# Kernel tuning notes

Hardware: AMD Instinct MI355X
Metric: run time of the kernel (lower is better)

The kernel has to match this reference:

```python
import jax, jax.numpy as jnp
import numpy as np

MARGIN = 40.0


def setup_inputs() -> dict:
    key = jax.random.key(0)
    k1, k2 = jax.random.split(key)
    feat = jax.random.normal(k1, (4096, 512), dtype=jnp.float32)
    targets = jax.random.randint(k2, (4096,), 0, 64, dtype=jnp.int64)
    return {"feat": feat, "targets": targets}


def reference(feat, targets):
    # corr: (n, n) Gram matrix of features
    corr = feat @ feat.T
    # mask[i, j] = True if same class
    mask = targets[:, None] == targets[None, :]
    big = jnp.asarray(jnp.finfo(corr.dtype).max, corr.dtype)
    # per-row min over positives, max over negatives
    corr_ap = jnp.min(jnp.where(mask, corr, big), axis=1)
    corr_an = jnp.max(jnp.where(mask, -big, corr), axis=1)
    # MarginRankingLoss(margin=40) with y = 1: mean(relu(-(ap - an) + margin))
    loss = jnp.mean(jax.nn.relu(corr_an - corr_ap + MARGIN))
    return loss
```

## Files before the change

kernel.cpp:

```cpp
#include <hip/hip_runtime.h>
#include <float.h>
#include <stdint.h>


#define N_ROWS 4096
#define D_K    512
#define BT     128
#define BK     64
#define NTB    (N_ROWS / BT)
#define NTILES (NTB * (NTB + 1) / 2)
#define MARGIN 40.0f
#define FOLD_BLOCKS 16

typedef __bf16 bf16_t;
typedef bf16_t bf16x8 __attribute__((ext_vector_type(8)));
typedef float  floatx4 __attribute__((ext_vector_type(4)));
typedef unsigned short ushort_t;
typedef ushort_t ushortx8 __attribute__((ext_vector_type(8)));

#define GLOAD_LDS16(g, l)                                        \
    __builtin_amdgcn_global_load_lds(                            \
        (const __attribute__((address_space(1))) void*)(g),      \
        (__attribute__((address_space(3))) void*)(l), 16, 0, 0)

__device__ __forceinline__ ushort_t f2bf_rne(float x) {
    uint32_t u = __builtin_bit_cast(uint32_t, x);
    return (ushort_t)((u + 0x7FFFu + ((u >> 16) & 1u)) >> 16);
}

__global__ __launch_bounds__(256) void cast_kernel(
    const float* __restrict__ f, ushort_t* __restrict__ o,
    int* __restrict__ counter)
{
    const int gid = blockIdx.x * 256 + threadIdx.x;
    if (gid == 0) *counter = 0;

    const int i = gid * 8;
    const float4 v0 = *(const float4*)(f + i);
    const float4 v1 = *(const float4*)(f + i + 4);
    ushortx8 r;
    r[0] = f2bf_rne(v0.x); r[1] = f2bf_rne(v0.y);
    r[2] = f2bf_rne(v0.z); r[3] = f2bf_rne(v0.w);
    r[4] = f2bf_rne(v1.x); r[5] = f2bf_rne(v1.y);
    r[6] = f2bf_rne(v1.z); r[7] = f2bf_rne(v1.w);
    *(ushortx8*)(o + i) = r;
}

__global__ __launch_bounds__(512, 6) void gram_mfma_kernel(
    const ushort_t* __restrict__ fb, const int* __restrict__ tgt,
    float* __restrict__ ap_part, float* __restrict__ an_part)
{
    __shared__ __align__(16) ushort_t As[BT * BK];
    __shared__ __align__(16) ushort_t Bs[BT * BK];
    __shared__ int tgI[BT];
    __shared__ int tgJ[BT];

    float* apRed  = (float*)As;
    float* anRed  = apRed  + 4 * BT;
    float* apRedT = anRed  + 4 * BT;
    float* anRedT = apRedT + 2 * BT;

    int bi = 0, rem = blockIdx.x;
    while (rem >= NTB - bi) { rem -= NTB - bi; ++bi; }
    const int bj = bi + rem;

    const int tid  = threadIdx.x;
    const int i0   = bi * BT;
    const int j0   = bj * BT;
    const int lane = tid & 63;
    const int wave = tid >> 6;
    const int wr   = wave >> 2;
    const int wc   = wave & 3;
    const int lr   = lane & 15;
    const int lg   = lane >> 4;
    const int sw   = lr & 7;

    if (tid < BT)            tgI[tid]      = tgt[i0 + tid];
    else if (tid < 2 * BT)   tgJ[tid - BT] = tgt[j0 + tid - BT];

    const int srow = tid >> 3;
    const int schk = (tid & 7) ^ (srow & 7);
    const size_t gA0 = (size_t)(i0 + srow) * D_K + schk * 8;
    const size_t gB0 = (size_t)(j0 + srow) * D_K + schk * 8;
    const size_t gHi = (size_t)64 * D_K;
    char* AsB = (char*)As;
    char* BsB = (char*)Bs;

    floatx4 acc[4][2];
#pragma unroll
    for (int a = 0; a < 4; ++a)
#pragma unroll
        for (int b = 0; b < 2; ++b) acc[a][b] = (floatx4)0.0f;

    for (int k0 = 0; k0 < D_K; k0 += BK) {
        GLOAD_LDS16(fb + gA0 + k0,       AsB + tid * 16);
        GLOAD_LDS16(fb + gA0 + gHi + k0, AsB + 8192 + tid * 16);
        GLOAD_LDS16(fb + gB0 + k0,       BsB + tid * 16);
        GLOAD_LDS16(fb + gB0 + gHi + k0, BsB + 8192 + tid * 16);
        __syncthreads();

#pragma unroll
        for (int h = 0; h < 2; ++h) {
            bf16x8 af[4], bfr[2];
            const int pc = ((h * 4 + lg) ^ sw) * 8;
#pragma unroll
            for (int rg = 0; rg < 4; ++rg)
                af[rg] = *(const bf16x8*)(As + (wr * 64 + rg * 16 + lr) * BK + pc);
#pragma unroll
            for (int cg = 0; cg < 2; ++cg)
                bfr[cg] = *(const bf16x8*)(Bs + (wc * 32 + cg * 16 + lr) * BK + pc);
#pragma unroll
            for (int rg = 0; rg < 4; ++rg)
#pragma unroll
                for (int cg = 0; cg < 2; ++cg)
                    acc[rg][cg] = __builtin_amdgcn_mfma_f32_16x16x32_bf16(
                        af[rg], bfr[cg], acc[rg][cg], 0, 0, 0);
        }
        __syncthreads();
    }

    int tj[2];
#pragma unroll
    for (int cg = 0; cg < 2; ++cg) tj[cg] = tgJ[wc * 32 + cg * 16 + lr];

    float apT[2], anT[2];
#pragma unroll
    for (int cg = 0; cg < 2; ++cg) { apT[cg] = FLT_MAX; anT[cg] = -FLT_MAX; }

#pragma unroll
    for (int rg = 0; rg < 4; ++rg) {
#pragma unroll
        for (int r = 0; r < 4; ++r) {
            const int rloc = wr * 64 + rg * 16 + lg * 4 + r;
            const int ti = tgI[rloc];
            float vap = FLT_MAX, van = -FLT_MAX;
#pragma unroll
            for (int cg = 0; cg < 2; ++cg) {
                const float v = acc[rg][cg][r];
                if (ti == tj[cg]) { vap = fminf(vap, v); apT[cg] = fminf(apT[cg], v); }
                else              { van = fmaxf(van, v); anT[cg] = fmaxf(anT[cg], v); }
            }
#pragma unroll
            for (int m = 1; m < 16; m <<= 1) {
                vap = fminf(vap, __shfl_xor(vap, m));
                van = fmaxf(van, __shfl_xor(van, m));
            }
            if (lr == 0) { apRed[wc * BT + rloc] = vap; anRed[wc * BT + rloc] = van; }
        }
    }
#pragma unroll
    for (int cg = 0; cg < 2; ++cg) {
        float vap = apT[cg], van = anT[cg];
        vap = fminf(vap, __shfl_xor(vap, 16)); van = fmaxf(van, __shfl_xor(van, 16));
        vap = fminf(vap, __shfl_xor(vap, 32)); van = fmaxf(van, __shfl_xor(van, 32));
        if (lg == 0) {
            apRedT[wr * BT + wc * 32 + cg * 16 + lr] = vap;
            anRedT[wr * BT + wc * 32 + cg * 16 + lr] = van;
        }
    }
    __syncthreads();

    if (tid < BT) {
        const float ap = fminf(fminf(apRed[0 * BT + tid], apRed[1 * BT + tid]),
                               fminf(apRed[2 * BT + tid], apRed[3 * BT + tid]));
        const float an = fmaxf(fmaxf(anRed[0 * BT + tid], anRed[1 * BT + tid]),
                               fmaxf(anRed[2 * BT + tid], anRed[3 * BT + tid]));
        ap_part[(size_t)bj * N_ROWS + i0 + tid] = ap;
        an_part[(size_t)bj * N_ROWS + i0 + tid] = an;
        if (bi != bj) {
            ap_part[(size_t)bi * N_ROWS + j0 + tid] =
                fminf(apRedT[0 * BT + tid], apRedT[1 * BT + tid]);
            an_part[(size_t)bi * N_ROWS + j0 + tid] =
                fmaxf(anRedT[0 * BT + tid], anRedT[1 * BT + tid]);
        }
    }
}

__global__ __launch_bounds__(256) void fold_kernel(
    const float* __restrict__ ap_part, const float* __restrict__ an_part,
    float* __restrict__ blk_sum, int* __restrict__ counter,
    float* __restrict__ out)
{
    __shared__ float sred[4];
    const int tid = threadIdx.x;
    const int row = blockIdx.x * 256 + tid;
    const int lane = tid & 63;
    const int wave = tid >> 6;

    float ap = FLT_MAX, an = -FLT_MAX;
#pragma unroll 8
    for (int s = 0; s < NTB; ++s) {
        ap = fminf(ap, ap_part[(size_t)s * N_ROWS + row]);
        an = fmaxf(an, an_part[(size_t)s * N_ROWS + row]);
    }
    const float v = an - ap + MARGIN;
    float local = (v > 0.0f) ? v : 0.0f;
#pragma unroll
    for (int m = 32; m >= 1; m >>= 1) local += __shfl_down(local, m);
    if (lane == 0) sred[wave] = local;
    __syncthreads();

    if (tid == 0) {
        blk_sum[blockIdx.x] = sred[0] + sred[1] + sred[2] + sred[3];
        __threadfence();
        if (atomicAdd(counter, 1) == FOLD_BLOCKS - 1) {
            __threadfence();
            float s = 0.0f;
#pragma unroll
            for (int b = 0; b < FOLD_BLOCKS; ++b) s += blk_sum[b];
            out[0] = s * (1.0f / N_ROWS);
        }
    }
}

extern "C" void kernel_launch(void* const* d_in, const int* in_sizes, int n_in,
                              void* d_out, int out_size, void* d_ws, size_t ws_size,
                              hipStream_t stream)
{
    const float* feat = (const float*)d_in[0];
    const int*   tgt  = (const int*)d_in[1];

    ushort_t* fb      = (ushort_t*)d_ws;
    float*    ap_part = (float*)(fb + (size_t)N_ROWS * D_K);
    float*    an_part = ap_part + (size_t)NTB * N_ROWS;
    float*    blk_sum = an_part + (size_t)NTB * N_ROWS;
    int*      counter = (int*)(blk_sum + FOLD_BLOCKS);

    cast_kernel<<<(N_ROWS * D_K) / (256 * 8), 256, 0, stream>>>(feat, fb, counter);
    gram_mfma_kernel<<<NTILES, 512, 0, stream>>>(fb, tgt, ap_part, an_part);
    fold_kernel<<<FOLD_BLOCKS, 256, 0, stream>>>(ap_part, an_part, blk_sum,
                                                 counter, (float*)d_out);
}
```

Measured before the change: 86.40 us.

## Double-buffer LDS tiles and fold reduction into gram kernel via atomics

Double-buffers the A/B LDS tiles so the next K-slice's global-to-LDS loads are issued before the MFMAs on the current slice, leaving one barrier per iteration. It replaces the per-tile partial arrays and the separate fold kernel with monotonic-encoded atomicMin/atomicMax on per-row min/max. The last block, found through a global counter, computes the final loss. This doubles LDS use, lowers the occupancy hint from 6 to 4, and adds global atomics, but removes one kernel launch and the partial-array traffic.

Measured after the change: 95.54 us. +10.6%, slower.

```diff
diff --git a/kernel.cpp b/kernel.cpp
--- a/kernel.cpp
+++ b/kernel.cpp
@@ -9,8 +9,8 @@
 #define BK     64
 #define NTB    (N_ROWS / BT)
 #define NTILES (NTB * (NTB + 1) / 2)
+#define NITER  (D_K / BK)
 #define MARGIN 40.0f
-#define FOLD_BLOCKS 16
 
 typedef __bf16 bf16_t;
 typedef bf16_t bf16x8 __attribute__((ext_vector_type(8)));
@@ -28,12 +28,23 @@
     return (ushort_t)((u + 0x7FFFu + ((u >> 16) & 1u)) >> 16);
 }
 
+__device__ __forceinline__ unsigned int f2mono(float x) {
+    uint32_t u = __builtin_bit_cast(uint32_t, x);
+    return (u & 0x80000000u) ? ~u : (u | 0x80000000u);
+}
+__device__ __forceinline__ float mono2f(unsigned int m) {
+    uint32_t u = (m & 0x80000000u) ? (m ^ 0x80000000u) : ~m;
+    return __builtin_bit_cast(float, u);
+}
+
 __global__ __launch_bounds__(256) void cast_kernel(
     const float* __restrict__ f, ushort_t* __restrict__ o,
+    unsigned int* __restrict__ ap_m, unsigned int* __restrict__ an_m,
     int* __restrict__ counter)
 {
     const int gid = blockIdx.x * 256 + threadIdx.x;
     if (gid == 0) *counter = 0;
+    if (gid < N_ROWS) { ap_m[gid] = 0xFFFFFFFFu; an_m[gid] = 0u; }
 
     const int i = gid * 8;
     const float4 v0 = *(const float4*)(f + i);
@@ -46,14 +57,16 @@
     *(ushortx8*)(o + i) = r;
 }
 
-__global__ __launch_bounds__(512, 6) void gram_mfma_kernel(
+__global__ __launch_bounds__(512, 4) void gram_mfma_kernel(
     const ushort_t* __restrict__ fb, const int* __restrict__ tgt,
-    float* __restrict__ ap_part, float* __restrict__ an_part)
+    unsigned int* __restrict__ ap_m, unsigned int* __restrict__ an_m,
+    int* __restrict__ counter, float* __restrict__ out)
 {
-    __shared__ __align__(16) ushort_t As[BT * BK];
-    __shared__ __align__(16) ushort_t Bs[BT * BK];
+    __shared__ __align__(16) ushort_t As[2][BT * BK];
+    __shared__ __align__(16) ushort_t Bs[2][BT * BK];
     __shared__ int tgI[BT];
     __shared__ int tgJ[BT];
+    __shared__ int s_last;
 
     float* apRed  = (float*)As;
     float* anRed  = apRed  + 4 * BT;
@@ -83,8 +96,14 @@
     const size_t gA0 = (size_t)(i0 + srow) * D_K + schk * 8;
     const size_t gB0 = (size_t)(j0 + srow) * D_K + schk * 8;
     const size_t gHi = (size_t)64 * D_K;
-    char* AsB = (char*)As;
-    char* BsB = (char*)Bs;
+
+#define STAGE(buf, kk) do {                                          \
+        char* aD = (char*)As[buf]; char* bD = (char*)Bs[buf];        \
+        GLOAD_LDS16(fb + gA0 + (kk),       aD + tid * 16);           \
+        GLOAD_LDS16(fb + gA0 + gHi + (kk), aD + 8192 + tid * 16);    \
+        GLOAD_LDS16(fb + gB0 + (kk),       bD + tid * 16);           \
+        GLOAD_LDS16(fb + gB0 + gHi + (kk), bD + 8192 + tid * 16);    \
+    } while (0)
 
     floatx4 acc[4][2];
 #pragma unroll
@@ -92,23 +111,26 @@
 #pragma unroll
         for (int b = 0; b < 2; ++b) acc[a][b] = (floatx4)0.0f;
 
-    for (int k0 = 0; k0 < D_K; k0 += BK) {
-        GLOAD_LDS16(fb + gA0 + k0,       AsB + tid * 16);
-        GLOAD_LDS16(fb + gA0 + gHi + k0, AsB + 8192 + tid * 16);
-        GLOAD_LDS16(fb + gB0 + k0,       BsB + tid * 16);
-        GLOAD_LDS16(fb + gB0 + gHi + k0, BsB + 8192 + tid * 16);
-        __syncthreads();
-
+    STAGE(0, 0);
+    __syncthreads();
+
+    int cur = 0;
+#pragma unroll
+    for (int t = 0; t < NITER; ++t) {
+        if (t + 1 < NITER) STAGE(cur ^ 1, (t + 1) * BK);
+
+        const ushort_t* Acur = As[cur];
+        const ushort_t* Bcur = Bs[cur];
 #pragma unroll
         for (int h = 0; h < 2; ++h) {
             bf16x8 af[4], bfr[2];
             const int pc = ((h * 4 + lg) ^ sw) * 8;
 #pragma unroll
             for (int rg = 0; rg < 4; ++rg)
-                af[rg] = *(const bf16x8*)(As + (wr * 64 + rg * 16 + lr) * BK + pc);
+                af[rg] = *(const bf16x8*)(Acur + (wr * 64 + rg * 16 + lr) * BK + pc);
 #pragma unroll
             for (int cg = 0; cg < 2; ++cg)
-                bfr[cg] = *(const bf16x8*)(Bs + (wc * 32 + cg * 16 + lr) * BK + pc);
+                bfr[cg] = *(const bf16x8*)(Bcur + (wc * 32 + cg * 16 + lr) * BK + pc);
 #pragma unroll
             for (int rg = 0; rg < 4; ++rg)
 #pragma unroll
@@ -116,7 +138,10 @@
                     acc[rg][cg] = __builtin_amdgcn_mfma_f32_16x16x32_bf16(
                         af[rg], bfr[cg], acc[rg][cg], 0, 0, 0);
         }
-        __syncthreads();
+        if (t + 1 < NITER) {
+            __syncthreads();
+            cur ^= 1;
+        }
     }
 
     int tj[2];
@@ -165,52 +190,47 @@
                                fminf(apRed[2 * BT + tid], apRed[3 * BT + tid]));
         const float an = fmaxf(fmaxf(anRed[0 * BT + tid], anRed[1 * BT + tid]),
                                fmaxf(anRed[2 * BT + tid], anRed[3 * BT + tid]));
-        ap_part[(size_t)bj * N_ROWS + i0 + tid] = ap;
-        an_part[(size_t)bj * N_ROWS + i0 + tid] = an;
+        atomicMin(ap_m + i0 + tid, f2mono(ap));
+        atomicMax(an_m + i0 + tid, f2mono(an));
         if (bi != bj) {
-            ap_part[(size_t)bi * N_ROWS + j0 + tid] =
-                fminf(apRedT[0 * BT + tid], apRedT[1 * BT + tid]);
-            an_part[(size_t)bi * N_ROWS + j0 + tid] =
-                fmaxf(anRedT[0 * BT + tid], anRedT[1 * BT + tid]);
-        }
-    }
-}
-
-__global__ __launch_bounds__(256) void fold_kernel(
-    const float* __restrict__ ap_part, const float* __restrict__ an_part,
-    float* __restrict__ blk_sum, int* __restrict__ counter,
-    float* __restrict__ out)
-{
-    __shared__ float sred[4];
-    const int tid = threadIdx.x;
-    const int row = blockIdx.x * 256 + tid;
-    const int lane = tid & 63;
-    const int wave = tid >> 6;
-
-    float ap = FLT_MAX, an = -FLT_MAX;
-#pragma unroll 8
-    for (int s = 0; s < NTB; ++s) {
-        ap = fminf(ap, ap_part[(size_t)s * N_ROWS + row]);
-        an = fmaxf(an, an_part[(size_t)s * N_ROWS + row]);
-    }
-    const float v = an - ap + MARGIN;
-    float local = (v > 0.0f) ? v : 0.0f;
-#pragma unroll
-    for (int m = 32; m >= 1; m >>= 1) local += __shfl_down(local, m);
-    if (lane == 0) sred[wave] = local;
-    __syncthreads();
-
+            atomicMin(ap_m + j0 + tid,
+                      f2mono(fminf(apRedT[0 * BT + tid], apRedT[1 * BT + tid])));
+            atomicMax(an_m + j0 + tid,
+                      f2mono(fmaxf(anRedT[0 * BT + tid], anRedT[1 * BT + tid])));
+        }
+    }
+
+    __syncthreads();
     if (tid == 0) {
-        blk_sum[blockIdx.x] = sred[0] + sred[1] + sred[2] + sred[3];
         __threadfence();
-        if (atomicAdd(counter, 1) == FOLD_BLOCKS - 1) {
-            __threadfence();
+        s_last = (atomicAdd(counter, 1) == NTILES - 1) ? 1 : 0;
+    }
+    __syncthreads();
+
+    if (s_last) {
+        __threadfence();
+        float local = 0.0f;
+#pragma unroll
+        for (int q = 0; q < N_ROWS / 512; ++q) {
+            const int r = q * 512 + tid;
+            const float ap = mono2f(atomicOr(ap_m + r, 0u));
+            const float an = mono2f(atomicOr(an_m + r, 0u));
+            const float v  = an - ap + MARGIN;
+            local += (v > 0.0f) ? v : 0.0f;
+        }
+#pragma unroll
+        for (int m = 32; m >= 1; m >>= 1) local += __shfl_down(local, m);
+        float* fin = (float*)Bs;
+        if (lane == 0) fin[wave] = local;
+        __syncthreads();
+        if (tid == 0) {
             float s = 0.0f;
 #pragma unroll
-            for (int b = 0; b < FOLD_BLOCKS; ++b) s += blk_sum[b];
+            for (int w = 0; w < 8; ++w) s += fin[w];
             out[0] = s * (1.0f / N_ROWS);
         }
     }
+#undef STAGE
 }
 
 extern "C" void kernel_launch(void* const* d_in, const int* in_sizes, int n_in,
@@ -220,14 +240,13 @@
     const float* feat = (const float*)d_in[0];
     const int*   tgt  = (const int*)d_in[1];
 
-    ushort_t* fb      = (ushort_t*)d_ws;
-    float*    ap_part = (float*)(fb + (size_t)N_ROWS * D_K);
-    float*    an_part = ap_part + (size_t)NTB * N_ROWS;
-    float*    blk_sum = an_part + (size_t)NTB * N_ROWS;
-    int*      counter = (int*)(blk_sum + FOLD_BLOCKS);
-
-    cast_kernel<<<(N_ROWS * D_K) / (256 * 8), 256, 0, stream>>>(feat, fb, counter);
-    gram_mfma_kernel<<<NTILES, 512, 0, stream>>>(fb, tgt, ap_part, an_part);
-    fold_kernel<<<FOLD_BLOCKS, 256, 0, stream>>>(ap_part, an_part, blk_sum,
-                                                 counter, (float*)d_out);
-}
+    ushort_t*     fb   = (ushort_t*)d_ws;
+    unsigned int* ap_m = (unsigned int*)(fb + (size_t)N_ROWS * D_K);
+    unsigned int* an_m = ap_m + N_ROWS;
+    int*          counter = (int*)(an_m + N_ROWS);
+
+    cast_kernel<<<(N_ROWS * D_K) / (256 * 8), 256, 0, stream>>>(
+        feat, fb, ap_m, an_m, counter);
+    gram_mfma_kernel<<<NTILES, 512, 0, stream>>>(
+        fb, tgt, ap_m, an_m, counter, (float*)d_out);
+}
```
